# Kernel optimization log

Hardware: AMD Instinct MI355X
Metric: run time of the kernel (lower is better)

## Reference

```python
import jax, jax.numpy as jnp
import numpy as np

N_NODES = 50000
N_EDGES = 600000
EMBED_DIM = 128


def setup_inputs() -> dict:
    key = jax.random.key(0)
    k1, k2 = jax.random.split(key)
    x = jax.random.normal(k1, (N_NODES, EMBED_DIM), dtype=jnp.float32)
    edge_index = jax.random.randint(k2, (2, N_EDGES), 0, N_NODES, dtype=jnp.int64)
    bias = jnp.zeros((EMBED_DIM,), dtype=jnp.float32)
    return {"x": x, "edge_index": edge_index, "bias": bias}


def reference(x, edge_index, bias):
    # init_embedding is Identity (disable_init_embedding=True)
    init_embeds = x
    n = x.shape[0]
    # add_self_loops
    loops = jnp.arange(n, dtype=edge_index.dtype)
    row = jnp.concatenate([edge_index[0], loops])  # source nodes
    col = jnp.concatenate([edge_index[1], loops])  # destination nodes
    # degree of destination nodes
    deg = jax.ops.segment_sum(jnp.ones_like(col, dtype=x.dtype), col, num_segments=n)
    deg_inv_sqrt = jnp.where(deg > 0, jax.lax.rsqrt(jnp.maximum(deg, 1e-20)), 0.0)
    # symmetric GCN normalization per edge
    norm = deg_inv_sqrt[row] * deg_inv_sqrt[col]  # [E+N]
    # message: gather source features, scale, scatter-add into destinations
    msg = norm[:, None] * x[row]  # [E+N, D]
    out = jax.ops.segment_sum(msg, col, num_segments=n) + bias
    return (out, init_embeds)
```

## Files before the change

### kernel.cpp

```cpp
#include <hip/hip_runtime.h>

#define D 128
#define B 256
#define WMAX 64
#define SPILL_MAX 8192

typedef float vfloat4 __attribute__((ext_vector_type(4)));


__device__ __forceinline__ unsigned short f2bf(float f) {
    unsigned u = __float_as_uint(f);
    u = u + 0x7FFFu + ((u >> 16) & 1u);
    return (unsigned short)(u >> 16);
}

__device__ __forceinline__ vfloat4 bf2f4(uint2 v) {
    vfloat4 r;
    r.x = __uint_as_float(v.x << 16);
    r.y = __uint_as_float(v.x & 0xffff0000u);
    r.z = __uint_as_float(v.y << 16);
    r.w = __uint_as_float(v.y & 0xffff0000u);
    return r;
}

__global__ void k_prep(const float* __restrict__ x, float* __restrict__ out2,
                       uint2* __restrict__ xb, int* __restrict__ cursor,
                       int* __restrict__ spillCnt, int n) {
    int gid = blockIdx.x * blockDim.x + threadIdx.x;
    if (gid == 0) *spillCnt = 0;
    if (gid < n) cursor[gid] = 0;
    if (gid >= n * 32) return;
    vfloat4 xv = reinterpret_cast<const vfloat4*>(x)[gid];
    __builtin_nontemporal_store(xv, reinterpret_cast<vfloat4*>(out2) + gid);
    uint2 b;
    b.x = (unsigned)f2bf(xv.x) | ((unsigned)f2bf(xv.y) << 16);
    b.y = (unsigned)f2bf(xv.z) | ((unsigned)f2bf(xv.w) << 16);
    xb[gid] = b;
}

__global__ void k_place_ell(const int* __restrict__ row, const int* __restrict__ col,
                            int* __restrict__ cursor, int* __restrict__ ssrc,
                            int2* __restrict__ spill, int* __restrict__ spillCnt, int e) {
    int i = blockIdx.x * blockDim.x + threadIdx.x;
    if (i >= e) return;
    int r = row[i];
    int c = col[i];
    int pos = atomicAdd(&cursor[c], 1);
    if (pos < WMAX) {
        ssrc[(size_t)c * WMAX + pos] = r;
    } else {
        int s = atomicAdd(spillCnt, 1);
        if (s < SPILL_MAX) spill[s] = make_int2(r, c);
    }
}

__global__ void k_agg_ell(const uint2* __restrict__ xb, const float* __restrict__ bias,
                          const int* __restrict__ cursor, const int* __restrict__ ssrc,
                          float* __restrict__ out, int n) {
    int gid = blockIdx.x * blockDim.x + threadIdx.x;
    if (gid >= n * 32) return;
    int node = gid >> 5;
    int q    = gid & 31;

    int cnt = cursor[node];
    int m   = min(cnt, WMAX);
    const int* sp = ssrc + (size_t)node * WMAX;

    vfloat4 a0 = {0.f, 0.f, 0.f, 0.f};
    vfloat4 a1 = a0, a2 = a0, a3 = a0;

    int j = 0;
    for (; j + 4 <= m; j += 4) {
        int r0 = sp[j + 0], r1 = sp[j + 1], r2 = sp[j + 2], r3 = sp[j + 3];
        uint2 v0 = xb[(size_t)r0 * 32 + q];
        uint2 v1 = xb[(size_t)r1 * 32 + q];
        uint2 v2 = xb[(size_t)r2 * 32 + q];
        uint2 v3 = xb[(size_t)r3 * 32 + q];
        float w0 = rsqrtf((float)cursor[r0] + 1.0f);
        float w1 = rsqrtf((float)cursor[r1] + 1.0f);
        float w2 = rsqrtf((float)cursor[r2] + 1.0f);
        float w3 = rsqrtf((float)cursor[r3] + 1.0f);
        a0 += w0 * bf2f4(v0);
        a1 += w1 * bf2f4(v1);
        a2 += w2 * bf2f4(v2);
        a3 += w3 * bf2f4(v3);
    }
    for (; j < m; ++j) {
        int r = sp[j];
        uint2 v = xb[(size_t)r * 32 + q];
        float w = rsqrtf((float)cursor[r] + 1.0f);
        a0 += w * bf2f4(v);
    }

    float dc = rsqrtf((float)cnt + 1.0f);
    vfloat4 xc = bf2f4(xb[(size_t)node * 32 + q]);
    vfloat4 bv = reinterpret_cast<const vfloat4*>(bias)[q];
    vfloat4 ov = bv + dc * (a0 + a1 + a2 + a3 + dc * xc);

    __builtin_nontemporal_store(ov, reinterpret_cast<vfloat4*>(out) + (size_t)node * 32 + q);
}

__global__ void k_spill(const float* __restrict__ x, const int* __restrict__ cursor,
                        const int2* __restrict__ spill, const int* __restrict__ spillCnt,
                        float* __restrict__ out) {
    int t = blockIdx.x * blockDim.x + threadIdx.x;
    int cnt = min(*spillCnt, SPILL_MAX);
    int edge = t >> 5;
    if (edge >= cnt) return;
    int q = t & 31;
    int2 p = spill[edge];
    float w = rsqrtf((float)cursor[p.x] + 1.0f) * rsqrtf((float)cursor[p.y] + 1.0f);
    vfloat4 xv = reinterpret_cast<const vfloat4*>(x)[(size_t)p.x * 32 + q];
    float* o = out + (size_t)p.y * D + q * 4;
    unsafeAtomicAdd(o + 0, w * xv.x);
    unsafeAtomicAdd(o + 1, w * xv.y);
    unsafeAtomicAdd(o + 2, w * xv.z);
    unsafeAtomicAdd(o + 3, w * xv.w);
}


__global__ void k_zero(int* __restrict__ degInt, int n) {
    int i = blockIdx.x * blockDim.x + threadIdx.x;
    if (i < n) degInt[i] = 0;
}

__global__ void k_count(const int* __restrict__ col, int* __restrict__ degInt, int e) {
    int i = blockIdx.x * blockDim.x + threadIdx.x;
    if (i < e) atomicAdd(&degInt[col[i]], 1);
}

__global__ void k_scan1(const int* __restrict__ degInt, int* __restrict__ off,
                        int* __restrict__ bsum, int n) {
    __shared__ int sm[B];
    int i = blockIdx.x * B + threadIdx.x;
    int v = (i < n) ? degInt[i] : 0;
    sm[threadIdx.x] = v;
    __syncthreads();
    for (int s = 1; s < B; s <<= 1) {
        int t = (threadIdx.x >= (unsigned)s) ? sm[threadIdx.x - s] : 0;
        __syncthreads();
        sm[threadIdx.x] += t;
        __syncthreads();
    }
    if (i < n) off[i] = sm[threadIdx.x] - v;
    if (threadIdx.x == B - 1) bsum[blockIdx.x] = sm[B - 1];
}

__global__ void k_scan2(int* __restrict__ bsum, int nb) {
    __shared__ int sm[B];
    int v = (threadIdx.x < (unsigned)nb) ? bsum[threadIdx.x] : 0;
    sm[threadIdx.x] = v;
    __syncthreads();
    for (int s = 1; s < B; s <<= 1) {
        int t = (threadIdx.x >= (unsigned)s) ? sm[threadIdx.x - s] : 0;
        __syncthreads();
        sm[threadIdx.x] += t;
        __syncthreads();
    }
    if (threadIdx.x < (unsigned)nb) bsum[threadIdx.x] = sm[threadIdx.x] - v;
}

__global__ void k_scan3(int* __restrict__ off, const int* __restrict__ bsum,
                        const int* __restrict__ degInt, float* __restrict__ dis,
                        int* __restrict__ cursor, int n, int e) {
    int i = blockIdx.x * B + threadIdx.x;
    if (i < n) {
        int o = off[i] + bsum[blockIdx.x];
        off[i] = o;
        cursor[i] = o;
        dis[i] = rsqrtf((float)degInt[i] + 1.0f);
    }
    if (i == 0) off[n] = e;
}

__global__ void k_place_pairs(const int* __restrict__ row, const int* __restrict__ col,
                              const float* __restrict__ dis, int* __restrict__ cursor,
                              int2* __restrict__ pairs, int e) {
    int i = blockIdx.x * blockDim.x + threadIdx.x;
    if (i >= e) return;
    int r = row[i];
    int c = col[i];
    float w = dis[r];
    int pos = atomicAdd(&cursor[c], 1);
    pairs[pos] = make_int2(r, __float_as_int(w));
}

__global__ void k_aggregate_pairs(const float* __restrict__ x, const float* __restrict__ bias,
                                  const float* __restrict__ dis, const int* __restrict__ off,
                                  const int2* __restrict__ pairs, float* __restrict__ out,
                                  float* __restrict__ out2, int n) {
    int gid = blockIdx.x * blockDim.x + threadIdx.x;
    if (gid >= n * 32) return;
    int node = gid >> 5;
    int q    = gid & 31;
    const vfloat4* x4 = reinterpret_cast<const vfloat4*>(x);
    int j   = off[node];
    int end = off[node + 1];
    vfloat4 a0 = {0.f, 0.f, 0.f, 0.f};
    vfloat4 a1 = a0, a2 = a0, a3 = a0;
    for (; j + 4 <= end; j += 4) {
        int2 p0 = pairs[j + 0];
        int2 p1 = pairs[j + 1];
        int2 p2 = pairs[j + 2];
        int2 p3 = pairs[j + 3];
        vfloat4 v0 = x4[(size_t)p0.x * 32 + q];
        vfloat4 v1 = x4[(size_t)p1.x * 32 + q];
        vfloat4 v2 = x4[(size_t)p2.x * 32 + q];
        vfloat4 v3 = x4[(size_t)p3.x * 32 + q];
        a0 += __int_as_float(p0.y) * v0;
        a1 += __int_as_float(p1.y) * v1;
        a2 += __int_as_float(p2.y) * v2;
        a3 += __int_as_float(p3.y) * v3;
    }
    for (; j < end; ++j) {
        int2 p = pairs[j];
        a0 += __int_as_float(p.y) * x4[(size_t)p.x * 32 + q];
    }
    float dc = dis[node];
    vfloat4 xc = x4[(size_t)node * 32 + q];
    vfloat4 bv = reinterpret_cast<const vfloat4*>(bias)[q];
    vfloat4 ov = bv + dc * (a0 + a1 + a2 + a3 + dc * xc);
    __builtin_nontemporal_store(ov, reinterpret_cast<vfloat4*>(out)  + (size_t)node * 32 + q);
    __builtin_nontemporal_store(xc, reinterpret_cast<vfloat4*>(out2) + (size_t)node * 32 + q);
}


extern "C" void kernel_launch(void* const* d_in, const int* in_sizes, int n_in,
                              void* d_out, int out_size, void* d_ws, size_t ws_size,
                              hipStream_t stream) {
    const float* x    = (const float*)d_in[0];
    const int*   idx  = (const int*)d_in[1];
    const float* bias = (const float*)d_in[2];

    const int n = in_sizes[0] / D;
    const int e = in_sizes[1] / 2;

    const int* row = idx;
    const int* col = idx + e;

    float* out  = (float*)d_out;
    float* out2 = (float*)d_out + (size_t)n * D;

    const int nbN = (n + B - 1) / B;
    const int nbE = (e + B - 1) / B;
    const int aggB = (n * 32 + B - 1) / B;

    char* p0 = (char*)d_ws;
    int*  cursor  = (int*)p0;                        p0 += (size_t)n * 4;
    int*  spillCnt= (int*)p0;                        p0 += 16;
    int2* spill   = (int2*)p0;                       p0 += (size_t)SPILL_MAX * 8;
    p0 = (char*)(((uintptr_t)p0 + 15) & ~(uintptr_t)15);
    uint2* xb     = (uint2*)p0;                      p0 += (size_t)n * 32 * 8;
    int*  ssrc    = (int*)p0;                        p0 += (size_t)n * WMAX * 4;
    size_t need_ell = (size_t)(p0 - (char*)d_ws);

    if (ws_size >= need_ell) {
        k_prep     <<<aggB, B, 0, stream>>>(x, out2, xb, cursor, spillCnt, n);
        k_place_ell<<<nbE,  B, 0, stream>>>(row, col, cursor, ssrc, spill, spillCnt, e);
        k_agg_ell  <<<aggB, B, 0, stream>>>(xb, bias, cursor, ssrc, out, n);
        k_spill    <<<(SPILL_MAX * 32) / B, B, 0, stream>>>(x, cursor, spill, spillCnt, out);
        return;
    }

    char* p = (char*)d_ws;
    int*   degInt = (int*)p;            p += (size_t)n * 4;
    int*   cur2   = (int*)p;            p += (size_t)n * 4;
    int*   off    = (int*)p;            p += (size_t)(n + 1) * 4;
    int*   bsum   = (int*)p;            p += 256 * 4;
    float* dis    = (float*)p;          p += (size_t)n * 4;
    p = (char*)(((uintptr_t)p + 15) & ~(uintptr_t)15);
    int2*  pairs  = (int2*)p;

    k_zero <<<nbN, B, 0, stream>>>(degInt, n);
    k_count<<<nbE, B, 0, stream>>>(col, degInt, e);
    k_scan1<<<nbN, B, 0, stream>>>(degInt, off, bsum, n);
    k_scan2<<<1,   B, 0, stream>>>(bsum, nbN);
    k_scan3<<<nbN, B, 0, stream>>>(off, bsum, degInt, dis, cur2, n, e);
    k_place_pairs<<<nbE, B, 0, stream>>>(row, col, dis, cur2, pairs, e);
    k_aggregate_pairs<<<aggB, B, 0, stream>>>(x, bias, dis, off, pairs, out, out2, n);
}
```

Baseline: 84.33 us.

## Fold spill handling into ELL aggregation and batch edge placement per thread

Removes the separate spill kernel launch and instead has the aggregation kernel scan the spill list for nodes whose in-degree exceeds WMAX, which also drops the float atomics on the output. Edge placement now processes four edges per thread with a grid-stride layout so multiple atomics are in flight per thread. Index arithmetic switches from size_t to int in a couple of spots. The spill scan is linear in spill count per overflowing node, which is cheap only because overflow is rare with this degree distribution.

```diff
diff --git a/kernel.cpp b/kernel.cpp
--- a/kernel.cpp
+++ b/kernel.cpp
@@ -4,6 +4,7 @@
 #define B 256
 #define WMAX 64
 #define SPILL_MAX 8192
+#define UPL 4
 
 typedef float vfloat4 __attribute__((ext_vector_type(4)));
 
@@ -41,21 +42,35 @@
 __global__ void k_place_ell(const int* __restrict__ row, const int* __restrict__ col,
                             int* __restrict__ cursor, int* __restrict__ ssrc,
                             int2* __restrict__ spill, int* __restrict__ spillCnt, int e) {
-    int i = blockIdx.x * blockDim.x + threadIdx.x;
-    if (i >= e) return;
-    int r = row[i];
-    int c = col[i];
-    int pos = atomicAdd(&cursor[c], 1);
-    if (pos < WMAX) {
-        ssrc[(size_t)c * WMAX + pos] = r;
-    } else {
-        int s = atomicAdd(spillCnt, 1);
-        if (s < SPILL_MAX) spill[s] = make_int2(r, c);
+    int t = blockIdx.x * blockDim.x + threadIdx.x;
+    int T = gridDim.x * blockDim.x;
+
+    int r[UPL], c[UPL], p[UPL];
+#pragma unroll
+    for (int u = 0; u < UPL; ++u) {
+        int i = t + u * T;
+        bool v = (i < e);
+        r[u] = v ? row[i] : -1;
+        c[u] = v ? col[i] : 0;
+    }
+#pragma unroll
+    for (int u = 0; u < UPL; ++u)
+        p[u] = (r[u] >= 0) ? atomicAdd(&cursor[c[u]], 1) : 0;
+#pragma unroll
+    for (int u = 0; u < UPL; ++u) {
+        if (r[u] < 0) continue;
+        if (p[u] < WMAX) {
+            ssrc[c[u] * WMAX + p[u]] = r[u];
+        } else {
+            int s = atomicAdd(spillCnt, 1);
+            if (s < SPILL_MAX) spill[s] = make_int2(r[u], c[u]);
+        }
     }
 }
 
 __global__ void k_agg_ell(const uint2* __restrict__ xb, const float* __restrict__ bias,
                           const int* __restrict__ cursor, const int* __restrict__ ssrc,
+                          const int2* __restrict__ spill, const int* __restrict__ spillCnt,
                           float* __restrict__ out, int n) {
     int gid = blockIdx.x * blockDim.x + threadIdx.x;
     if (gid >= n * 32) return;
@@ -64,7 +79,7 @@
 
     int cnt = cursor[node];
     int m   = min(cnt, WMAX);
-    const int* sp = ssrc + (size_t)node * WMAX;
+    const int* sp = ssrc + node * WMAX;
 
     vfloat4 a0 = {0.f, 0.f, 0.f, 0.f};
     vfloat4 a1 = a0, a2 = a0, a3 = a0;
@@ -92,30 +107,23 @@
         a0 += w * bf2f4(v);
     }
 
+    if (cnt > WMAX) {
+        int sc = min(*spillCnt, SPILL_MAX);
+        for (int s = 0; s < sc; ++s) {
+            int2 pr = spill[s];
+            if (pr.y == node) {
+                float w = rsqrtf((float)cursor[pr.x] + 1.0f);
+                a0 += w * bf2f4(xb[(size_t)pr.x * 32 + q]);
+            }
+        }
+    }
+
     float dc = rsqrtf((float)cnt + 1.0f);
     vfloat4 xc = bf2f4(xb[(size_t)node * 32 + q]);
     vfloat4 bv = reinterpret_cast<const vfloat4*>(bias)[q];
     vfloat4 ov = bv + dc * (a0 + a1 + a2 + a3 + dc * xc);
 
     __builtin_nontemporal_store(ov, reinterpret_cast<vfloat4*>(out) + (size_t)node * 32 + q);
-}
-
-__global__ void k_spill(const float* __restrict__ x, const int* __restrict__ cursor,
-                        const int2* __restrict__ spill, const int* __restrict__ spillCnt,
-                        float* __restrict__ out) {
-    int t = blockIdx.x * blockDim.x + threadIdx.x;
-    int cnt = min(*spillCnt, SPILL_MAX);
-    int edge = t >> 5;
-    if (edge >= cnt) return;
-    int q = t & 31;
-    int2 p = spill[edge];
-    float w = rsqrtf((float)cursor[p.x] + 1.0f) * rsqrtf((float)cursor[p.y] + 1.0f);
-    vfloat4 xv = reinterpret_cast<const vfloat4*>(x)[(size_t)p.x * 32 + q];
-    float* o = out + (size_t)p.y * D + q * 4;
-    unsafeAtomicAdd(o + 0, w * xv.x);
-    unsafeAtomicAdd(o + 1, w * xv.y);
-    unsafeAtomicAdd(o + 2, w * xv.z);
-    unsafeAtomicAdd(o + 3, w * xv.w);
 }
 
 
@@ -255,10 +263,10 @@
     size_t need_ell = (size_t)(p0 - (char*)d_ws);
 
     if (ws_size >= need_ell) {
+        const int plB = (e + B * UPL - 1) / (B * UPL);
         k_prep     <<<aggB, B, 0, stream>>>(x, out2, xb, cursor, spillCnt, n);
-        k_place_ell<<<nbE,  B, 0, stream>>>(row, col, cursor, ssrc, spill, spillCnt, e);
-        k_agg_ell  <<<aggB, B, 0, stream>>>(xb, bias, cursor, ssrc, out, n);
-        k_spill    <<<(SPILL_MAX * 32) / B, B, 0, stream>>>(x, cursor, spill, spillCnt, out);
+        k_place_ell<<<plB,  B, 0, stream>>>(row, col, cursor, ssrc, spill, spillCnt, e);
+        k_agg_ell  <<<aggB, B, 0, stream>>>(xb, bias, cursor, ssrc, spill, spillCnt, out, n);
         return;
     }
 
```

Result: faster. 81.91 us (-2.9%).
